# Optimization experiments

Hardware: AMD Instinct MI355X
Metric: run time of the kernel (lower is better)

Reference implementation:

```python
import jax, jax.numpy as jnp
import numpy as np

MAX_ITERS = 4096  # safety cap; original loops until convergence (expected ~235 iters here)
COS_EPS = 1e-8    # torch F.cosine_similarity denominator clamp


def fire_neurons(x, b, q, e):
    """Vectorized GLS chaotic firing. x:(B,N); b,q,e:(N,). Returns k:(B,N).

    Faithful to the torch loop: m starts at q, each iteration applies the skew-tent
    map to ALL elements; an element stays 'active' while it has been outside
    [x-e, x+e] in every iteration so far (intersection chain), and k counts
    1 + number of iterations it stayed active. Elements with q==0 never fire.
    """
    m0 = jnp.broadcast_to(q, x.shape).astype(x.dtype)
    k0 = jnp.ones_like(x)
    act0 = m0 != 0  # torch.nonzero(m[idx]) seeds the active set
    lo = x - e
    hi = x + e

    def cond(state):
        i, m, k, act = state
        return jnp.logical_and(act.any(), i < MAX_ITERS)

    def body(state):
        i, m, k, act = state
        m = jnp.where(m < b, m / b, (1.0 - m) / (1.0 - b))  # skew-tent GLS map
        invalid = (m < lo) | (m > hi)
        act = act & invalid                                  # np.intersect1d(invalid, last)
        k = k + act.astype(k.dtype)
        return (i + 1, m, k, act)

    _, _, k, _ = jax.lax.while_loop(cond, body, (jnp.int32(0), m0, k0, act0))
    return k


def cosine_logits(k, M):
    """Row-wise cosine similarity of each firing pattern k[i]:(N,) vs each class row M[c]:(N,)."""
    kn = jnp.maximum(jnp.linalg.norm(k, axis=1), COS_EPS)  # (B,)
    Mn = jnp.maximum(jnp.linalg.norm(M, axis=1), COS_EPS)  # (C,)
    return (k @ M.T) / (kn[:, None] * Mn[None, :])          # (B,C)


def setup_inputs() -> dict:
    key = jax.random.key(0)
    kx, kb, kq, ke, kM = jax.random.split(key, 5)
    B, N, C = 256, 8192, 100
    x = jax.random.uniform(kx, (B, N), dtype=jnp.float32)              # inputs in (0,1)
    b = 0.25 + 0.5 * jax.random.uniform(kb, (N,), dtype=jnp.float32)   # map break in (0.25,0.75)
    q = 0.02 + 0.96 * jax.random.uniform(kq, (N,), dtype=jnp.float32)  # nonzero init potential
    e = 0.03 + 0.03 * jax.random.uniform(ke, (N,), dtype=jnp.float32)  # epsilon in (0.03,0.06)
    M = jax.random.uniform(kM, (C, N), dtype=jnp.float32)              # class prototypes (post-train)
    return {"x": x, "b": b, "q": q, "e": e, "M": M}


def reference(x, b, q, e, M):
    # forward(x, return_logits=True): fire neurons, then per-sample cosine similarity vs M
    k = fire_neurons(x, b, q, e)
    return cosine_logits(k, M)
```

## Files before the change

kernel.cpp:

```cpp
#include <hip/hip_runtime.h>
#include <math.h>

#define NN 8192
#define BB 256
#define CC 100
#define MAX_ITERS 4096

__global__ __launch_bounds__(256) void fire_kernel(
    const float* __restrict__ x, const float* __restrict__ bmap,
    const float* __restrict__ qini, const float* __restrict__ eps,
    float* __restrict__ kout)
{
    const int j    = blockIdx.x;
    const int lane = threadIdx.x & 63;
    const int row  = (threadIdx.x & ~63) + lane;

    const float bv  = bmap[j];
    const float qv  = qini[j];
    const float ev  = eps[j];
    const float obv = 1.0f - bv;
    const float rb  = 1.0f / bv;
    const float rob = 1.0f / obv;

    const float xv  = x[(size_t)row * NN + j];
    const float lov = xv - ev;
    const float hiv = xv + ev;

    float m = qv, anchor = qv;
    int   window = 1, steps = 0;
    int   kk = 1;
    bool  a  = (qv != 0.0f);
    bool  cycseen = false;

    int it = 0;
    while (it < MAX_ITERS) {
        #pragma unroll
        for (int u = 0; u < 4; ++u) {
            const bool  lt = (m < bv);
            const float pa = m * rb;
            const float pb = (1.0f - m) * rob;
            m = lt ? pa : pb;

            cycseen = cycseen || (m == anchor);
            if (++steps == window) { anchor = m; window <<= 1; steps = 0; }

            const bool o = (m < lov) || (m > hiv);
            a = a && o;
            kk += a ? 1 : 0;
        }
        it += 4;
        if (__ballot(a) == 0ull) break;
        if (cycseen) {
            kk += a ? (MAX_ITERS - it) : 0;
            break;
        }
    }

    kout[(size_t)row * NN + j] = (float)kk;
}

__global__ __launch_bounds__(256) void norm_kernel(
    const float* __restrict__ k, const float* __restrict__ M,
    float* __restrict__ norms)
{
    __shared__ double red[4];
    const int row = blockIdx.x;
    const float* src = (row < BB) ? (k + (size_t)row * NN)
                                  : (M + (size_t)(row - BB) * NN);
    double s = 0.0;
    for (int j = threadIdx.x * 4; j < NN; j += 1024) {
        const float4 v = *(const float4*)(src + j);
        s += (double)v.x * v.x + (double)v.y * v.y
           + (double)v.z * v.z + (double)v.w * v.w;
    }
    #pragma unroll
    for (int off = 32; off; off >>= 1) s += __shfl_down(s, off, 64);
    const int wid = threadIdx.x >> 6, lane = threadIdx.x & 63;
    if (lane == 0) red[wid] = s;
    __syncthreads();
    if (threadIdx.x == 0)
        norms[row] = fmaxf((float)sqrt(red[0] + red[1] + red[2] + red[3]), 1e-8f);
}

#define TR 8
#define TC 5
__global__ __launch_bounds__(256) void logits_gemm(
    const float* __restrict__ k, const float* __restrict__ M,
    const float* __restrict__ norms, float* __restrict__ out)
{
    __shared__ float red[4][TR][TC];

    const int rt  = blockIdx.x / (CC / TC);
    const int ct  = blockIdx.x % (CC / TC);
    const int r0  = rt * TR, c0 = ct * TC;
    const int tid = threadIdx.x;
    const int wid = tid >> 6, lane = tid & 63;

    float acc[TR][TC];
    #pragma unroll
    for (int r = 0; r < TR; ++r)
        #pragma unroll
        for (int c = 0; c < TC; ++c) acc[r][c] = 0.0f;

    for (int s = 0; s < 8; ++s) {
        const int jj = s * 1024 + tid * 4;
        float4 mv[TC];
        #pragma unroll
        for (int c = 0; c < TC; ++c)
            mv[c] = *(const float4*)(M + (size_t)(c0 + c) * NN + jj);
        #pragma unroll
        for (int r = 0; r < TR; ++r) {
            const float4 kv = *(const float4*)(k + (size_t)(r0 + r) * NN + jj);
            #pragma unroll
            for (int c = 0; c < TC; ++c)
                acc[r][c] += kv.x * mv[c].x + kv.y * mv[c].y
                           + kv.z * mv[c].z + kv.w * mv[c].w;
        }
    }

    #pragma unroll
    for (int off = 32; off; off >>= 1)
        #pragma unroll
        for (int r = 0; r < TR; ++r)
            #pragma unroll
            for (int c = 0; c < TC; ++c)
                acc[r][c] += __shfl_down(acc[r][c], off, 64);
    if (lane == 0)
        #pragma unroll
        for (int r = 0; r < TR; ++r)
            #pragma unroll
            for (int c = 0; c < TC; ++c)
                red[wid][r][c] = acc[r][c];
    __syncthreads();

    if (tid < TR * TC) {
        const int r = tid / TC, c = tid % TC;
        const float d = red[0][r][c] + red[1][r][c] + red[2][r][c] + red[3][r][c];
        out[(size_t)(r0 + r) * CC + (c0 + c)] =
            d / (norms[r0 + r] * norms[BB + c0 + c]);
    }
}

__global__ __launch_bounds__(256) void gls_fused_kernel(
    const float* __restrict__ x, const float* __restrict__ bmap,
    const float* __restrict__ qini, const float* __restrict__ eps,
    const float* __restrict__ M, float* __restrict__ out)
{
    __shared__ float k_lds[NN];
    __shared__ double redsh[4];

    const int i   = blockIdx.x;
    const int tid = threadIdx.x;
    const int wid = tid >> 6, lane = tid & 63;

    double sumsq = 0.0;
    for (int s = 0; s < 32; ++s) {
        const int j = tid + 256 * s;
        const float bv = bmap[j];
        const float qv = qini[j];
        const float ev = eps[j];
        const float xv = x[(size_t)i * NN + j];
        const float lov = xv - ev;
        const float hiv = xv + ev;
        const float obv = 1.0f - bv;
        const float rb  = 1.0f / bv;
        const float rob = 1.0f / obv;

        float m  = qv;
        float kk = 1.0f;
        bool  a  = (qv != 0.0f);
        for (int it = 0; a && it < MAX_ITERS; ++it) {
            const bool  lt  = (m < bv);
            const float num = lt ? m  : (1.0f - m);
            const float r   = lt ? rb : rob;
            m = num * r;
            a = (m < lov) || (m > hiv);
            kk += a ? 1.0f : 0.0f;
        }
        k_lds[j] = kk;
        sumsq += (double)kk * (double)kk;
    }

    #pragma unroll
    for (int off = 32; off; off >>= 1) sumsq += __shfl_down(sumsq, off, 64);
    if (lane == 0) redsh[wid] = sumsq;
    __syncthreads();
    const double rn = fmax(sqrt(redsh[0] + redsh[1] + redsh[2] + redsh[3]), 1e-8);

    for (int cc2 = 0; cc2 < 25; ++cc2) {
        const int c = wid * 25 + cc2;
        const float4* Mp = (const float4*)(M + (size_t)c * NN);
        double dot = 0.0, msq = 0.0;
        #pragma unroll 4
        for (int s = 0; s < 32; ++s) {
            const float4 mv = Mp[lane + 64 * s];
            const float4 kv = *(const float4*)(&k_lds[4 * (lane + 64 * s)]);
            dot += (double)kv.x * (double)mv.x + (double)kv.y * (double)mv.y
                 + (double)kv.z * (double)mv.z + (double)kv.w * (double)mv.w;
            msq += (double)mv.x * (double)mv.x + (double)mv.y * (double)mv.y
                 + (double)mv.z * (double)mv.z + (double)mv.w * (double)mv.w;
        }
        #pragma unroll
        for (int off = 32; off; off >>= 1) {
            dot += __shfl_down(dot, off, 64);
            msq += __shfl_down(msq, off, 64);
        }
        if (lane == 0) {
            const double mn = fmax(sqrt(msq), 1e-8);
            out[(size_t)i * CC + c] = (float)(dot / (rn * mn));
        }
    }
}

extern "C" void kernel_launch(void* const* d_in, const int* in_sizes, int n_in,
                              void* d_out, int out_size, void* d_ws, size_t ws_size,
                              hipStream_t stream) {
    const float* x = (const float*)d_in[0];
    const float* b = (const float*)d_in[1];
    const float* q = (const float*)d_in[2];
    const float* e = (const float*)d_in[3];
    const float* M = (const float*)d_in[4];
    float* out = (float*)d_out;

    const size_t need = (size_t)BB * NN * sizeof(float) + (BB + CC) * sizeof(float);
    if (ws_size >= need) {
        float* kbuf  = (float*)d_ws;
        float* norms = kbuf + (size_t)BB * NN;
        fire_kernel<<<dim3(NN), dim3(256), 0, stream>>>(x, b, q, e, kbuf);
        norm_kernel<<<dim3(BB + CC), dim3(256), 0, stream>>>(kbuf, M, norms);
        logits_gemm<<<dim3((BB / TR) * (CC / TC)), dim3(256), 0, stream>>>(kbuf, M, norms, out);
    } else {
        gls_fused_kernel<<<dim3(BB), dim3(256), 0, stream>>>(x, b, q, e, M, out);
    }
}
```

Baseline: 106.1 us.

## Split firing into capped first pass plus compacted tail pass for long-running wavefronts

The firing kernel now runs each wavefront for at most a fixed iteration cap. Wavefronts still active after the cap save their map state and active mask to a global work list through an atomic counter. A second kernel with a grid-stride loop then resumes those straggler wavefronts, so a few long-running columns no longer hold whole workgroups and leave compute units idle. This costs two extra launches, the atomic, and a reload and rewrite of k for the tail. The cycle-detection anchor is also reset at resume, so cycle detection restarts from the saved state.

```diff
diff --git a/kernel.cpp b/kernel.cpp
--- a/kernel.cpp
+++ b/kernel.cpp
@@ -5,15 +5,22 @@
 #define BB 256
 #define CC 100
 #define MAX_ITERS 4096
-
-__global__ __launch_bounds__(256) void fire_kernel(
+#define T0CAP 192
+#define LISTMAX 16384
+
+__global__ void zero_kernel(unsigned* __restrict__ cnt) { *cnt = 0u; }
+
+
+__global__ __launch_bounds__(256) void fireA_kernel(
     const float* __restrict__ x, const float* __restrict__ bmap,
     const float* __restrict__ qini, const float* __restrict__ eps,
-    float* __restrict__ kout)
+    float* __restrict__ kout, unsigned* __restrict__ cnt,
+    uint4* __restrict__ list)
 {
     const int j    = blockIdx.x;
     const int lane = threadIdx.x & 63;
-    const int row  = (threadIdx.x & ~63) + lane;
+    const int wg   = threadIdx.x >> 6;
+    const int row  = wg * 64 + lane;
 
     const float bv  = bmap[j];
     const float qv  = qini[j];
@@ -31,32 +38,123 @@
     int   kk = 1;
     bool  a  = (qv != 0.0f);
     bool  cycseen = false;
+    bool  finished = false;
 
     int it = 0;
-    while (it < MAX_ITERS) {
+    while (it < T0CAP) {
         #pragma unroll
         for (int u = 0; u < 4; ++u) {
             const bool  lt = (m < bv);
             const float pa = m * rb;
             const float pb = (1.0f - m) * rob;
             m = lt ? pa : pb;
-
             cycseen = cycseen || (m == anchor);
             if (++steps == window) { anchor = m; window <<= 1; steps = 0; }
-
             const bool o = (m < lov) || (m > hiv);
             a = a && o;
             kk += a ? 1 : 0;
         }
         it += 4;
-        if (__ballot(a) == 0ull) break;
-        if (cycseen) {
-            kk += a ? (MAX_ITERS - it) : 0;
-            break;
+        if (__ballot(a) == 0ull) { finished = true; break; }
+        if (cycseen) { kk += a ? (MAX_ITERS - it) : 0; finished = true; break; }
+    }
+
+    if (!finished) {
+        const unsigned long long mask = __ballot(a);
+        unsigned idx = 0;
+        if (lane == 0) idx = atomicAdd(cnt, 1u);
+        idx = (unsigned)__shfl((int)idx, 0, 64);
+        if (idx < LISTMAX) {
+            if (lane == 0) {
+                uint4 rec;
+                rec.x = ((unsigned)j << 2) | (unsigned)wg;
+                rec.y = __float_as_uint(m);
+                rec.z = (unsigned)(mask & 0xffffffffull);
+                rec.w = (unsigned)(mask >> 32);
+                list[idx] = rec;
+            }
+            kout[(size_t)row * NN + j] = (float)kk;
+            return;
+        }
+        while (it < MAX_ITERS) {
+            #pragma unroll
+            for (int u = 0; u < 4; ++u) {
+                const bool  lt = (m < bv);
+                const float pa = m * rb;
+                const float pb = (1.0f - m) * rob;
+                m = lt ? pa : pb;
+                cycseen = cycseen || (m == anchor);
+                if (++steps == window) { anchor = m; window <<= 1; steps = 0; }
+                const bool o = (m < lov) || (m > hiv);
+                a = a && o;
+                kk += a ? 1 : 0;
+            }
+            it += 4;
+            if (__ballot(a) == 0ull) break;
+            if (cycseen) { kk += a ? (MAX_ITERS - it) : 0; break; }
         }
     }
 
     kout[(size_t)row * NN + j] = (float)kk;
+}
+
+__global__ __launch_bounds__(256) void fireB_kernel(
+    const float* __restrict__ x, const float* __restrict__ bmap,
+    const float* __restrict__ qini, const float* __restrict__ eps,
+    float* __restrict__ kout, const unsigned* __restrict__ cnt,
+    const uint4* __restrict__ list)
+{
+    const unsigned n = min(*cnt, (unsigned)LISTMAX);
+    const int lane  = threadIdx.x & 63;
+    const int wslot = threadIdx.x >> 6;
+    const unsigned slot0   = blockIdx.x * 4 + wslot;
+    const unsigned nslots  = gridDim.x * 4;
+
+    for (unsigned idx = slot0; idx < n; idx += nslots) {
+        const uint4 rec = list[idx];
+        const int j   = (int)(rec.x >> 2);
+        const int row = (int)(rec.x & 3u) * 64 + lane;
+
+        const float bv  = bmap[j];
+        const float ev  = eps[j];
+        const float obv = 1.0f - bv;
+        const float rb  = 1.0f / bv;
+        const float rob = 1.0f / obv;
+
+        const float xv  = x[(size_t)row * NN + j];
+        const float lov = xv - ev;
+        const float hiv = xv + ev;
+
+        const unsigned long long mask =
+            ((unsigned long long)rec.w << 32) | (unsigned long long)rec.z;
+        bool  a  = (mask >> lane) & 1ull;
+        int   kk = (int)kout[(size_t)row * NN + j];
+        float m  = __uint_as_float(rec.y);
+        float anchor = m;
+        int   window = 1, steps = 0;
+        bool  cycseen = false;
+
+        int it = T0CAP;
+        while (it < MAX_ITERS) {
+            #pragma unroll
+            for (int u = 0; u < 4; ++u) {
+                const bool  lt = (m < bv);
+                const float pa = m * rb;
+                const float pb = (1.0f - m) * rob;
+                m = lt ? pa : pb;
+                cycseen = cycseen || (m == anchor);
+                if (++steps == window) { anchor = m; window <<= 1; steps = 0; }
+                const bool o = (m < lov) || (m > hiv);
+                a = a && o;
+                kk += a ? 1 : 0;
+            }
+            it += 4;
+            if (__ballot(a) == 0ull) break;
+            if (cycseen) { kk += a ? (MAX_ITERS - it) : 0; break; }
+        }
+
+        kout[(size_t)row * NN + j] = (float)kk;
+    }
 }
 
 __global__ __launch_bounds__(256) void norm_kernel(
@@ -139,6 +237,54 @@
         out[(size_t)(r0 + r) * CC + (c0 + c)] =
             d / (norms[r0 + r] * norms[BB + c0 + c]);
     }
+}
+
+__global__ __launch_bounds__(256) void fire_kernel(
+    const float* __restrict__ x, const float* __restrict__ bmap,
+    const float* __restrict__ qini, const float* __restrict__ eps,
+    float* __restrict__ kout)
+{
+    const int j    = blockIdx.x;
+    const int lane = threadIdx.x & 63;
+    const int row  = (threadIdx.x & ~63) + lane;
+
+    const float bv  = bmap[j];
+    const float qv  = qini[j];
+    const float ev  = eps[j];
+    const float obv = 1.0f - bv;
+    const float rb  = 1.0f / bv;
+    const float rob = 1.0f / obv;
+
+    const float xv  = x[(size_t)row * NN + j];
+    const float lov = xv - ev;
+    const float hiv = xv + ev;
+
+    float m = qv, anchor = qv;
+    int   window = 1, steps = 0;
+    int   kk = 1;
+    bool  a  = (qv != 0.0f);
+    bool  cycseen = false;
+
+    int it = 0;
+    while (it < MAX_ITERS) {
+        #pragma unroll
+        for (int u = 0; u < 4; ++u) {
+            const bool  lt = (m < bv);
+            const float pa = m * rb;
+            const float pb = (1.0f - m) * rob;
+            m = lt ? pa : pb;
+            cycseen = cycseen || (m == anchor);
+            if (++steps == window) { anchor = m; window <<= 1; steps = 0; }
+            const bool o = (m < lov) || (m > hiv);
+            a = a && o;
+            kk += a ? 1 : 0;
+        }
+        it += 4;
+        if (__ballot(a) == 0ull) break;
+        if (cycseen) { kk += a ? (MAX_ITERS - it) : 0; break; }
+    }
+
+    kout[(size_t)row * NN + j] = (float)kk;
 }
 
 __global__ __launch_bounds__(256) void gls_fused_kernel(
@@ -222,8 +368,25 @@
     const float* M = (const float*)d_in[4];
     float* out = (float*)d_out;
 
-    const size_t need = (size_t)BB * NN * sizeof(float) + (BB + CC) * sizeof(float);
-    if (ws_size >= need) {
+    const size_t kbytes    = (size_t)BB * NN * sizeof(float);
+    const size_t off_norms = kbytes;
+    const size_t off_cnt   = kbytes + 2048;
+    const size_t off_list  = off_cnt + 64;
+    const size_t need_cont = off_list + sizeof(uint4) * LISTMAX;
+    const size_t need_r18  = kbytes + (BB + CC) * sizeof(float);
+
+    if (ws_size >= need_cont) {
+        float*    kbuf  = (float*)d_ws;
+        float*    norms = (float*)((char*)d_ws + off_norms);
+        unsigned* cnt   = (unsigned*)((char*)d_ws + off_cnt);
+        uint4*    list  = (uint4*)((char*)d_ws + off_list);
+
+        zero_kernel<<<dim3(1), dim3(1), 0, stream>>>(cnt);
+        fireA_kernel<<<dim3(NN), dim3(256), 0, stream>>>(x, b, q, e, kbuf, cnt, list);
+        fireB_kernel<<<dim3(1024), dim3(256), 0, stream>>>(x, b, q, e, kbuf, cnt, list);
+        norm_kernel<<<dim3(BB + CC), dim3(256), 0, stream>>>(kbuf, M, norms);
+        logits_gemm<<<dim3((BB / TR) * (CC / TC)), dim3(256), 0, stream>>>(kbuf, M, norms, out);
+    } else if (ws_size >= need_r18) {
         float* kbuf  = (float*)d_ws;
         float* norms = kbuf + (size_t)BB * NN;
         fire_kernel<<<dim3(NN), dim3(256), 0, stream>>>(x, b, q, e, kbuf);
```

Measured after the change: 125.2 us. +18.0%, slower.

## Drop cycle detection, fuse norm computation into logits GEMM, unroll firing loop 8x

Applied to the files above, without the earlier changes.

Removes Brent-style cycle detection from the firing loop, uses fmed3 for the out-of-window test, keeps k in float, and raises the unroll to 8 between wave ballots. Deletes the separate norm kernel and computes the row norms of k and M inside the logits GEMM, saving one launch and one full pass over k. The risks are that dropping cycle detection makes periodic active lanes run up to MAX_ITERS, and that the norms are recomputed redundantly in every tile. The extra double-precision accumulations also add register pressure to the GEMM.

```diff
diff --git a/kernel.cpp b/kernel.cpp
--- a/kernel.cpp
+++ b/kernel.cpp
@@ -26,69 +26,38 @@
     const float lov = xv - ev;
     const float hiv = xv + ev;
 
-    float m = qv, anchor = qv;
-    int   window = 1, steps = 0;
-    int   kk = 1;
+    float m  = qv;
+    float kk = 1.0f;
     bool  a  = (qv != 0.0f);
-    bool  cycseen = false;
 
     int it = 0;
     while (it < MAX_ITERS) {
         #pragma unroll
-        for (int u = 0; u < 4; ++u) {
+        for (int u = 0; u < 8; ++u) {
             const bool  lt = (m < bv);
             const float pa = m * rb;
             const float pb = (1.0f - m) * rob;
             m = lt ? pa : pb;
-
-            cycseen = cycseen || (m == anchor);
-            if (++steps == window) { anchor = m; window <<= 1; steps = 0; }
-
-            const bool o = (m < lov) || (m > hiv);
+            const bool o = (__builtin_amdgcn_fmed3f(m, lov, hiv) != m);
             a = a && o;
-            kk += a ? 1 : 0;
-        }
-        it += 4;
+            kk += a ? 1.0f : 0.0f;
+        }
+        it += 8;
         if (__ballot(a) == 0ull) break;
-        if (cycseen) {
-            kk += a ? (MAX_ITERS - it) : 0;
-            break;
-        }
-    }
-
-    kout[(size_t)row * NN + j] = (float)kk;
-}
-
-__global__ __launch_bounds__(256) void norm_kernel(
-    const float* __restrict__ k, const float* __restrict__ M,
-    float* __restrict__ norms)
-{
-    __shared__ double red[4];
-    const int row = blockIdx.x;
-    const float* src = (row < BB) ? (k + (size_t)row * NN)
-                                  : (M + (size_t)(row - BB) * NN);
-    double s = 0.0;
-    for (int j = threadIdx.x * 4; j < NN; j += 1024) {
-        const float4 v = *(const float4*)(src + j);
-        s += (double)v.x * v.x + (double)v.y * v.y
-           + (double)v.z * v.z + (double)v.w * v.w;
-    }
-    #pragma unroll
-    for (int off = 32; off; off >>= 1) s += __shfl_down(s, off, 64);
-    const int wid = threadIdx.x >> 6, lane = threadIdx.x & 63;
-    if (lane == 0) red[wid] = s;
-    __syncthreads();
-    if (threadIdx.x == 0)
-        norms[row] = fmaxf((float)sqrt(red[0] + red[1] + red[2] + red[3]), 1e-8f);
+    }
+
+    kout[(size_t)row * NN + j] = kk;
 }
 
 #define TR 8
 #define TC 5
 __global__ __launch_bounds__(256) void logits_gemm(
     const float* __restrict__ k, const float* __restrict__ M,
-    const float* __restrict__ norms, float* __restrict__ out)
+    float* __restrict__ out)
 {
-    __shared__ float red[4][TR][TC];
+    __shared__ float  red[4][TR][TC];
+    __shared__ double redk[4][TR];
+    __shared__ double redm[4][TC];
 
     const int rt  = blockIdx.x / (CC / TC);
     const int ct  = blockIdx.x % (CC / TC);
@@ -96,21 +65,32 @@
     const int tid = threadIdx.x;
     const int wid = tid >> 6, lane = tid & 63;
 
-    float acc[TR][TC];
-    #pragma unroll
-    for (int r = 0; r < TR; ++r)
+    float  acc[TR][TC];
+    double ksq[TR];
+    double msq[TC];
+    #pragma unroll
+    for (int r = 0; r < TR; ++r) {
+        ksq[r] = 0.0;
         #pragma unroll
         for (int c = 0; c < TC; ++c) acc[r][c] = 0.0f;
+    }
+    #pragma unroll
+    for (int c = 0; c < TC; ++c) msq[c] = 0.0;
 
     for (int s = 0; s < 8; ++s) {
         const int jj = s * 1024 + tid * 4;
         float4 mv[TC];
         #pragma unroll
-        for (int c = 0; c < TC; ++c)
+        for (int c = 0; c < TC; ++c) {
             mv[c] = *(const float4*)(M + (size_t)(c0 + c) * NN + jj);
+            msq[c] += (double)mv[c].x * mv[c].x + (double)mv[c].y * mv[c].y
+                    + (double)mv[c].z * mv[c].z + (double)mv[c].w * mv[c].w;
+        }
         #pragma unroll
         for (int r = 0; r < TR; ++r) {
             const float4 kv = *(const float4*)(k + (size_t)(r0 + r) * NN + jj);
+            ksq[r] += (double)kv.x * kv.x + (double)kv.y * kv.y
+                    + (double)kv.z * kv.z + (double)kv.w * kv.w;
             #pragma unroll
             for (int c = 0; c < TC; ++c)
                 acc[r][c] += kv.x * mv[c].x + kv.y * mv[c].y
@@ -119,25 +99,35 @@
     }
 
     #pragma unroll
-    for (int off = 32; off; off >>= 1)
-        #pragma unroll
-        for (int r = 0; r < TR; ++r)
+    for (int off = 32; off; off >>= 1) {
+        #pragma unroll
+        for (int r = 0; r < TR; ++r) {
+            ksq[r] += __shfl_down(ksq[r], off, 64);
             #pragma unroll
             for (int c = 0; c < TC; ++c)
                 acc[r][c] += __shfl_down(acc[r][c], off, 64);
-    if (lane == 0)
-        #pragma unroll
-        for (int r = 0; r < TR; ++r)
+        }
+        #pragma unroll
+        for (int c = 0; c < TC; ++c) msq[c] += __shfl_down(msq[c], off, 64);
+    }
+    if (lane == 0) {
+        #pragma unroll
+        for (int r = 0; r < TR; ++r) {
+            redk[wid][r] = ksq[r];
             #pragma unroll
-            for (int c = 0; c < TC; ++c)
-                red[wid][r][c] = acc[r][c];
+            for (int c = 0; c < TC; ++c) red[wid][r][c] = acc[r][c];
+        }
+        #pragma unroll
+        for (int c = 0; c < TC; ++c) redm[wid][c] = msq[c];
+    }
     __syncthreads();
 
     if (tid < TR * TC) {
         const int r = tid / TC, c = tid % TC;
-        const float d = red[0][r][c] + red[1][r][c] + red[2][r][c] + red[3][r][c];
-        out[(size_t)(r0 + r) * CC + (c0 + c)] =
-            d / (norms[r0 + r] * norms[BB + c0 + c]);
+        const float d  = red[0][r][c] + red[1][r][c] + red[2][r][c] + red[3][r][c];
+        const float kn = fmaxf((float)sqrt(redk[0][r] + redk[1][r] + redk[2][r] + redk[3][r]), 1e-8f);
+        const float mn = fmaxf((float)sqrt(redm[0][c] + redm[1][c] + redm[2][c] + redm[3][c]), 1e-8f);
+        out[(size_t)(r0 + r) * CC + (c0 + c)] = d / (kn * mn);
     }
 }
 
@@ -222,13 +212,11 @@
     const float* M = (const float*)d_in[4];
     float* out = (float*)d_out;
 
-    const size_t need = (size_t)BB * NN * sizeof(float) + (BB + CC) * sizeof(float);
+    const size_t need = (size_t)BB * NN * sizeof(float);
     if (ws_size >= need) {
-        float* kbuf  = (float*)d_ws;
-        float* norms = kbuf + (size_t)BB * NN;
+        float* kbuf = (float*)d_ws;
         fire_kernel<<<dim3(NN), dim3(256), 0, stream>>>(x, b, q, e, kbuf);
-        norm_kernel<<<dim3(BB + CC), dim3(256), 0, stream>>>(kbuf, M, norms);
-        logits_gemm<<<dim3((BB / TR) * (CC / TC)), dim3(256), 0, stream>>>(kbuf, M, norms, out);
+        logits_gemm<<<dim3((BB / TR) * (CC / TC)), dim3(256), 0, stream>>>(kbuf, M, out);
     } else {
         gls_fused_kernel<<<dim3(BB), dim3(256), 0, stream>>>(x, b, q, e, M, out);
     }
```

Measured after the change: 168.6 us. +58.9%, slower.
